# Optimization experiments

Hardware: AMD Instinct MI355X
Metric: run time of the kernel (lower is better)

The kernel has to match this reference:

```python
import jax, jax.numpy as jnp
import numpy as np

ITERATIONS = 20  # Resonator(iterations=20)
B, F, V, D = 128, 4, 2048, 4096


def _hardsign(x):
    # bipolar normalization used by MAP-VSA multiset(normalize=True); ties -> +1
    return jnp.where(x >= 0, 1.0, -1.0).astype(x.dtype)


def setup_inputs() -> dict:
    key = jax.random.key(0)
    k1, k2 = jax.random.split(key, 2)
    # bipolar codebooks: (F, V, D)
    codebooks = _hardsign(jax.random.normal(k1, (F, V, D), dtype=jnp.float32))
    # a realistic composite input: bind (elementwise product) of one codevector per factor
    idx = jax.random.randint(k2, (B, F), 0, V)                       # (B, F)
    chosen = codebooks[jnp.arange(F)[None, :], idx]                  # (B, F, D)
    inputs = jnp.prod(chosen, axis=1)                                # (B, D)
    # standard resonator init: normalized superposition of each codebook
    init_estimates = jnp.broadcast_to(
        _hardsign(jnp.sum(codebooks, axis=1)), (B, F, D)
    ).astype(jnp.float32)                                            # (B, F, D)
    return {"inputs": inputs, "init_estimates": init_estimates, "codebooks": codebooks}


def _resonator_step(inputs, est, codebooks):
    # est: (B, F, D). rolled stack over k=1..F-1 -> (B, F, F-1, D)
    f = est.shape[-2]
    rolled = jnp.stack([jnp.roll(est, k, axis=-2) for k in range(1, f)], axis=-2)
    inv_others = jnp.prod(rolled, axis=-2)          # multibind over dim -2 -> (B, F, D)
    new_est = inputs[:, None, :] * inv_others       # bind -> (B, F, D)
    sim = jnp.einsum('bfd,fvd->bfv', new_est, codebooks)   # similarity (activation='NONE')
    # multiset(codebooks, sim, normalize=True)
    return _hardsign(jnp.einsum('bfv,fvd->bfd', sim, codebooks))


def reference(inputs, init_estimates, codebooks):
    def body(carry, i):
        est, k, done = carry
        new = _resonator_step(inputs, est, codebooks)
        eq = jnp.all(new == est)          # convergence check (fixed point)
        k = jnp.where(done, k, i)
        return (new, k, done | eq), None

    carry0 = (init_estimates, jnp.int32(0), jnp.bool_(False))
    (est, k, _), _ = jax.lax.scan(body, carry0, jnp.arange(ITERATIONS, dtype=jnp.int32))
    # cleanup: argmax of |similarity| per factor (argmax_abs=True)
    sim = jnp.einsum('bfd,fvd->bfv', est, codebooks)
    outcome = jnp.argmax(jnp.abs(sim), axis=-1)     # (B, F) int indices
    return outcome, k
```

## Files before the change

kernel.cpp:

```cpp
#include <hip/hip_runtime.h>
#include <stdint.h>

#define B_    128
#define F_    4
#define V_    2048
#define D_    4096
#define DW    64
#define VW    32
#define ITERS 20
#define NKT   16

typedef _Float16 half8 __attribute__((ext_vector_type(8)));
typedef float   floatx4 __attribute__((ext_vector_type(4)));

__device__ __forceinline__ void pack16(const float* __restrict__ x,
                                       uint64_t* __restrict__ bits, int t) {
    const float4* p = (const float4*)x + (size_t)t * 4;
    uint32_t m = 0;
    #pragma unroll
    for (int j = 0; j < 4; ++j) {
        float4 v = p[j];
        m |= (__float_as_uint(v.x) >> 31) << (4 * j + 0);
        m |= (__float_as_uint(v.y) >> 31) << (4 * j + 1);
        m |= (__float_as_uint(v.z) >> 31) << (4 * j + 2);
        m |= (__float_as_uint(v.w) >> 31) << (4 * j + 3);
    }
    ((unsigned short*)bits)[t] = (unsigned short)m;
}

__global__ __launch_bounds__(256) void k_setup(
        const float* __restrict__ cb, const float* __restrict__ inite,
        const float* __restrict__ inputs,
        uint64_t* __restrict__ cb_bits, uint64_t* __restrict__ est_bits,
        uint64_t* __restrict__ in_bits,
        int* __restrict__ flags, int* __restrict__ keys) {
    int gtid = blockIdx.x * 256 + threadIdx.x;
    const int T = 512 * 256;
    const int ncb = (F_ * V_ * D_) / 16;
    for (int t = gtid; t < ncb; t += T) pack16(cb, cb_bits, t);
    pack16(inite, est_bits, gtid);
    if (gtid < (B_ * D_) / 16) pack16(inputs, in_bits, gtid);
    if (gtid < 32) flags[gtid] = 0;
    if (gtid < B_ * F_) keys[gtid] = 0;
}

__global__ void k_packT(const uint64_t* __restrict__ cb_bits,
                        uint64_t* __restrict__ cbT) {
    int vw = blockIdx.x, dwg = blockIdx.y, f = blockIdx.z;
    int lane = threadIdx.x & 63;
    int dw = dwg * 4 + (threadIdx.x >> 6);
    uint64_t w = cb_bits[((size_t)f * V_ + vw * 64 + lane) * DW + dw];
    uint64_t r = 0;
    for (int d2 = 0; d2 < 64; ++d2) {
        uint64_t m = __ballot((unsigned)((w >> d2) & 1));
        if (lane == d2) r = m;
    }
    cbT[((size_t)f * D_ + dw * 64 + lane) * VW + vw] = r;
}

__global__ __launch_bounds__(256) void k_sim(
        const uint64_t* __restrict__ cb_bits,
        const uint64_t* __restrict__ in_bits,
        const uint64_t* __restrict__ est_bits,
        _Float16* __restrict__ simf,
        const int* __restrict__ flags, int iter) {
    if (iter > 0 && flags[iter - 1] == 0) return;
    int vt = blockIdx.x, bt = blockIdx.y, f = blockIdx.z;
    int v0 = vt * 64, b0 = bt * 32;
    int tid = threadIdx.x;

    __shared__ __align__(16) ulonglong2 CB2[64 * 32];
    __shared__ __align__(16) ulonglong2 NB2[32 * 32];

    #pragma unroll
    for (int it = 0; it < 8; ++it) {
        int cq = it * 256 + tid;
        int r = cq >> 5, ch = cq & 31;
        const ulonglong2* src = (const ulonglong2*)(cb_bits + ((size_t)f * V_ + v0 + r) * DW);
        CB2[r * 32 + (ch ^ (r & 7))] = src[ch];
    }
    #pragma unroll
    for (int it = 0; it < 4; ++it) {
        int cq = it * 256 + tid;
        int r = cq >> 5, ch = cq & 31;
        int b = b0 + r;
        const ulonglong2* iv = (const ulonglong2*)(in_bits + (size_t)b * DW);
        const uint64_t* eb = est_bits + (size_t)b * F_ * DW;
        ulonglong2 i2 = iv[ch];
        ulonglong2 e0 = ((const ulonglong2*)(eb + 0 * DW))[ch];
        ulonglong2 e1 = ((const ulonglong2*)(eb + 1 * DW))[ch];
        ulonglong2 e2 = ((const ulonglong2*)(eb + 2 * DW))[ch];
        ulonglong2 e3 = ((const ulonglong2*)(eb + 3 * DW))[ch];
        ulonglong2 es = ((const ulonglong2*)(eb + (size_t)f * DW))[ch];
        ulonglong2 val;
        val.x = i2.x ^ e0.x ^ e1.x ^ e2.x ^ e3.x ^ es.x;
        val.y = i2.y ^ e0.y ^ e1.y ^ e2.y ^ e3.y ^ es.y;
        NB2[r * 32 + (ch ^ (r & 7))] = val;
    }
    __syncthreads();

    int vv = tid & 15, bb = tid >> 4;
    int svz = vv & 7, sbz = bb & 7;
    int pc[2][4];
    #pragma unroll
    for (int j = 0; j < 2; ++j)
        #pragma unroll
        for (int i = 0; i < 4; ++i) pc[j][i] = 0;

    #pragma unroll 4
    for (int ch = 0; ch < 32; ++ch) {
        ulonglong2 c[4], n[2];
        #pragma unroll
        for (int i = 0; i < 4; ++i)
            c[i] = CB2[(vv + 16 * i) * 32 + (ch ^ svz)];
        #pragma unroll
        for (int j = 0; j < 2; ++j)
            n[j] = NB2[(bb + 16 * j) * 32 + (ch ^ sbz)];
        #pragma unroll
        for (int j = 0; j < 2; ++j)
            #pragma unroll
            for (int i = 0; i < 4; ++i)
                pc[j][i] += __popcll(n[j].x ^ c[i].x) + __popcll(n[j].y ^ c[i].y);
    }
    #pragma unroll
    for (int j = 0; j < 2; ++j) {
        int b = b0 + bb + 16 * j;
        #pragma unroll
        for (int i = 0; i < 4; ++i) {
            int v = v0 + vv + 16 * i;
            simf[((size_t)f * B_ + b) * V_ + v] = (_Float16)(2048 - pc[j][i]);
        }
    }
}

__global__ __launch_bounds__(256) void k_gemm(
        const _Float16* __restrict__ simf,
        const uint64_t* __restrict__ cbT,
        uint64_t* __restrict__ est_bits,
        int* __restrict__ flags, int iter) {
    if (iter > 0 && flags[iter - 1] == 0) return;
    int nt = blockIdx.x, mt = blockIdx.y, f = blockIdx.z;
    int m0 = mt * 64, n0 = nt * 64;
    int tid = threadIdx.x;
    int lane = tid & 63, wave = tid >> 6;
    int lrow = lane & 15, lq = lane >> 4;
    int wm = wave & 1, wn = wave >> 1;

    __shared__ __align__(16) uint64_t Bb[64 * VW];
    __shared__ __align__(16) _Float16 As[64 * 128];
    __shared__ int bd;
    if (tid == 0) bd = 0;

    const uint64_t* bsrc = cbT + ((size_t)f * D_ + n0) * VW;
    #pragma unroll
    for (int p = 0; p < 4; ++p) {
        int chunk = p * 256 + tid;
        int dloc = chunk >> 4, cw = chunk & 15;
        ulonglong2 val = *(const ulonglong2*)&bsrc[dloc * VW + cw * 2];
        *(ulonglong2*)&Bb[dloc * VW + ((cw ^ (dloc & 15)) * 2)] = val;
    }

    const _Float16* Ab = simf + (size_t)f * B_ * V_ + (size_t)m0 * V_;
    int arow = tid >> 4, acol = tid & 15;
    half8 areg[4];
    #pragma unroll
    for (int p = 0; p < 4; ++p)
        areg[p] = *(const half8*)&Ab[(size_t)(p * 16 + arow) * V_ + acol * 8];

    floatx4 acc[2][2] = {};

    const uint64_t SPREAD = 0x1000200040008000ull;
    const uint64_t SMASK  = 0x8000800080008000ull;
    const uint64_t PONE   = 0x3C003C003C003C00ull;

    #pragma unroll 1
    for (int kt = 0; kt < NKT; ++kt) {
        __syncthreads();
        #pragma unroll
        for (int p = 0; p < 4; ++p)
            *(half8*)&As[(p * 16 + arow) * 128 + ((acol ^ arow) * 8)] = areg[p];
        if (kt + 1 < NKT) {
            #pragma unroll
            for (int p = 0; p < 4; ++p)
                areg[p] = *(const half8*)&Ab[(size_t)(p * 16 + arow) * V_ + (kt + 1) * 128 + acol * 8];
        }
        __syncthreads();

        ulonglong2 bw[2];
        #pragma unroll
        for (int nt2 = 0; nt2 < 2; ++nt2) {
            int dloc = wn * 32 + nt2 * 16 + lrow;
            bw[nt2] = *(const ulonglong2*)&Bb[dloc * VW + ((kt ^ (dloc & 15)) * 2)];
        }
        #pragma unroll
        for (int ks = 0; ks < 4; ++ks) {
            half8 af[2];
            #pragma unroll
            for (int mt2 = 0; mt2 < 2; ++mt2) {
                int row = wm * 32 + mt2 * 16 + lrow;
                af[mt2] = *(const half8*)&As[row * 128 + (((ks * 4 + lq) ^ lrow) * 8)];
            }
            half8 bfrag[2];
            #pragma unroll
            for (int nt2 = 0; nt2 < 2; ++nt2) {
                uint64_t w = (ks < 2) ? bw[nt2].x : bw[nt2].y;
                uint32_t byte = (uint32_t)(w >> ((((ks & 1) * 4 + lq)) * 8)) & 0xFFu;
                union { uint64_t q[2]; half8 h; } bu;
                bu.q[0] = (((uint64_t)(byte & 0xFu) * SPREAD) & SMASK) ^ PONE;
                bu.q[1] = (((uint64_t)(byte >> 4)   * SPREAD) & SMASK) ^ PONE;
                bfrag[nt2] = bu.h;
            }
            #pragma unroll
            for (int mt2 = 0; mt2 < 2; ++mt2)
                #pragma unroll
                for (int nt2 = 0; nt2 < 2; ++nt2)
                    acc[mt2][nt2] = __builtin_amdgcn_mfma_f32_16x16x32_f16(
                        af[mt2], bfrag[nt2], acc[mt2][nt2], 0, 0, 0);
        }
    }

    __syncthreads();
    unsigned char* S = (unsigned char*)As;
    #pragma unroll
    for (int mt2 = 0; mt2 < 2; ++mt2)
        #pragma unroll
        for (int nt2 = 0; nt2 < 2; ++nt2)
            #pragma unroll
            for (int r = 0; r < 4; ++r) {
                int row = wm * 32 + mt2 * 16 + lq * 4 + r;
                int col = wn * 32 + nt2 * 16 + lrow;
                S[row * 64 + col] = (acc[mt2][nt2][r] < 0.0f) ? 1 : 0;
            }
    __syncthreads();
    if (tid < 64) {
        const uint64_t* Sw = (const uint64_t*)S;
        uint64_t m = 0;
        #pragma unroll
        for (int j = 0; j < 8; ++j) {
            uint64_t w = Sw[tid * 8 + j];
            m |= ((w * 0x0102040810204080ull) >> 56) << (8 * j);
        }
        size_t widx = ((size_t)(m0 + tid) * F_ + f) * DW + nt;
        uint64_t old = est_bits[widx];
        est_bits[widx] = m;
        if (old != m) atomicOr(&bd, 1);
    }
    __syncthreads();
    if (tid == 0 && bd) atomicOr(&flags[iter], 1);
}

__global__ __launch_bounds__(256) void k_argmax(
        const uint64_t* __restrict__ cb_bits,
        const uint64_t* __restrict__ est_bits,
        int* __restrict__ keys) {
    int vt = blockIdx.x, f = blockIdx.y;
    int v0 = vt * 32;
    int tid = threadIdx.x;

    __shared__ __align__(16) ulonglong2 EB2[128 * 32];
    __shared__ __align__(16) ulonglong2 CBa[32 * 32];

    #pragma unroll
    for (int it = 0; it < 16; ++it) {
        int cq = it * 256 + tid;
        int r = cq >> 5, ch = cq & 31;
        const ulonglong2* src = (const ulonglong2*)(est_bits + ((size_t)r * F_ + f) * DW);
        EB2[r * 32 + (ch ^ (r & 7))] = src[ch];
    }
    #pragma unroll
    for (int it = 0; it < 4; ++it) {
        int cq = it * 256 + tid;
        int r = cq >> 5, ch = cq & 31;
        const ulonglong2* src = (const ulonglong2*)(cb_bits + ((size_t)f * V_ + v0 + r) * DW);
        CBa[r * 32 + (ch ^ (r & 7))] = src[ch];
    }
    __syncthreads();

    int vv = tid & 15, bb = tid >> 4;
    int svz = vv & 7, sbz = bb & 7;
    int pc[8][2];
    #pragma unroll
    for (int j = 0; j < 8; ++j) { pc[j][0] = 0; pc[j][1] = 0; }

    #pragma unroll 4
    for (int ch = 0; ch < 32; ++ch) {
        ulonglong2 c[2], n[8];
        #pragma unroll
        for (int i = 0; i < 2; ++i)
            c[i] = CBa[(vv + 16 * i) * 32 + (ch ^ svz)];
        #pragma unroll
        for (int j = 0; j < 8; ++j)
            n[j] = EB2[(bb + 16 * j) * 32 + (ch ^ sbz)];
        #pragma unroll
        for (int j = 0; j < 8; ++j)
            #pragma unroll
            for (int i = 0; i < 2; ++i)
                pc[j][i] += __popcll(n[j].x ^ c[i].x) + __popcll(n[j].y ^ c[i].y);
    }

    #pragma unroll
    for (int j = 0; j < 8; ++j) {
        int kj = (int)0x80000000;
        #pragma unroll
        for (int i = 0; i < 2; ++i) {
            int v = v0 + vv + 16 * i;
            int m = 2048 - pc[j][i]; if (m < 0) m = -m;
            int key = (m << 11) | (2047 - v);
            if (key > kj) kj = key;
        }
        #pragma unroll
        for (int s = 1; s < 16; s <<= 1) {
            int o = __shfl_xor(kj, s, 64);
            if (o > kj) kj = o;
        }
        if ((tid & 15) == 0)
            atomicMax(&keys[(size_t)(bb + 16 * j) * F_ + f], kj);
    }
}

__global__ void k_final(const int* __restrict__ keys, const int* __restrict__ flags,
                        int* __restrict__ out) {
    int tid = blockIdx.x * blockDim.x + threadIdx.x;
    if (tid < B_ * F_) out[tid] = 2047 - (keys[tid] & 0x7FF);
    if (tid == 0) {
        int k = ITERS - 1;
        for (int i = 0; i < ITERS; ++i) if (flags[i] == 0) { k = i; break; }
        out[B_ * F_] = k;
    }
}

extern "C" void kernel_launch(void* const* d_in, const int* in_sizes, int n_in,
                              void* d_out, int out_size, void* d_ws, size_t ws_size,
                              hipStream_t stream) {
    const float* inputs = (const float*)d_in[0];
    const float* inite  = (const float*)d_in[1];
    const float* cb     = (const float*)d_in[2];
    int* out = (int*)d_out;

    char* ws = (char*)d_ws;
    uint64_t* cb_bits  = (uint64_t*)ws;  ws += (size_t)F_ * V_ * DW * 8;
    uint64_t* cbT_bits = (uint64_t*)ws;  ws += (size_t)F_ * D_ * VW * 8;
    uint64_t* est_bits = (uint64_t*)ws;  ws += (size_t)B_ * F_ * DW * 8;
    uint64_t* in_bits  = (uint64_t*)ws;  ws += (size_t)B_ * DW * 8;
    _Float16* simf     = (_Float16*)ws;  ws += (size_t)F_ * B_ * V_ * 2;
    int*      flags    = (int*)ws;       ws += 32 * 4;
    int*      keys     = (int*)ws;       ws += B_ * F_ * 4;

    k_setup<<<512, 256, 0, stream>>>(cb, inite, inputs, cb_bits, est_bits,
                                     in_bits, flags, keys);
    k_packT<<<dim3(32, 16, 4), 256, 0, stream>>>(cb_bits, cbT_bits);

    for (int i = 0; i < ITERS; ++i) {
        k_sim<<<dim3(32, 4, 4), 256, 0, stream>>>(cb_bits, in_bits, est_bits, simf, flags, i);
        k_gemm<<<dim3(64, 2, 4), 256, 0, stream>>>(simf, cbT_bits, est_bits, flags, i);
    }
    k_argmax<<<dim3(64, 4), 256, 0, stream>>>(cb_bits, est_bits, keys);
    k_final<<<2, 256, 0, stream>>>(keys, flags, out);
}
```

Measured before the change: 950.4 us.

## Fuse resonator iterations into one persistent kernel with grid-wide barriers

Replaces the 40 per-iteration launches of the similarity and GEMM kernels with a single persistent kernel of 512 blocks. The blocks synchronise between phases through a hierarchical atomic-counter grid barrier. Shared estimate and similarity buffers are read and written with relaxed agent-scope atomics for cross-block visibility. This removes kernel launch gaps, but the per-iteration convergence early-exit is dropped and the spin barrier depends on all blocks being co-resident. The barrier also has a spin cap that could break synchronisation.

New measurement: 965.8 us. Within noise of the previous version (+1.6%).

```diff
diff --git a/kernel.cpp b/kernel.cpp
--- a/kernel.cpp
+++ b/kernel.cpp
@@ -9,9 +9,47 @@
 #define VW    32
 #define ITERS 20
 #define NKT   16
+#define NBLK  512
 
 typedef _Float16 half8 __attribute__((ext_vector_type(8)));
 typedef float   floatx4 __attribute__((ext_vector_type(4)));
+
+__device__ __forceinline__ uint64_t cload64(const uint64_t* p) {
+    return __hip_atomic_load(p, __ATOMIC_RELAXED, __HIP_MEMORY_SCOPE_AGENT);
+}
+__device__ __forceinline__ void cstore64(uint64_t* p, uint64_t v) {
+    __hip_atomic_store(p, v, __ATOMIC_RELAXED, __HIP_MEMORY_SCOPE_AGENT);
+}
+__device__ __forceinline__ ulonglong2 cload_u128(const uint64_t* p) {
+    ulonglong2 r;
+    r.x = cload64(p); r.y = cload64(p + 1);
+    return r;
+}
+__device__ __forceinline__ half8 cload_h8(const _Float16* p) {
+    union { uint64_t q[2]; half8 h; } u;
+    u.q[0] = cload64((const uint64_t*)p);
+    u.q[1] = cload64((const uint64_t*)p + 1);
+    return u.h;
+}
+
+__device__ __forceinline__ void xbar(int* bar, int gen) {
+    __syncthreads();
+    if (threadIdx.x == 0) {
+        int s = blockIdx.x & 15;
+        int t = __hip_atomic_fetch_add(&bar[s * 16], 1, __ATOMIC_RELAXED,
+                                       __HIP_MEMORY_SCOPE_AGENT);
+        if (t == gen * (NBLK / 16) - 1)
+            __hip_atomic_fetch_add(&bar[256], 1, __ATOMIC_RELAXED,
+                                   __HIP_MEMORY_SCOPE_AGENT);
+        int spins = 0;
+        while (__hip_atomic_load(&bar[256], __ATOMIC_RELAXED,
+                                 __HIP_MEMORY_SCOPE_AGENT) < gen * 16) {
+            __builtin_amdgcn_s_sleep(2);
+            if (++spins > (1 << 16)) break;
+        }
+    }
+    __syncthreads();
+}
 
 __device__ __forceinline__ void pack16(const float* __restrict__ x,
                                        uint64_t* __restrict__ bits, int t) {
@@ -58,195 +96,205 @@
     cbT[((size_t)f * D_ + dw * 64 + lane) * VW + vw] = r;
 }
 
-__global__ __launch_bounds__(256) void k_sim(
-        const uint64_t* __restrict__ cb_bits,
-        const uint64_t* __restrict__ in_bits,
-        const uint64_t* __restrict__ est_bits,
-        _Float16* __restrict__ simf,
-        const int* __restrict__ flags, int iter) {
-    if (iter > 0 && flags[iter - 1] == 0) return;
-    int vt = blockIdx.x, bt = blockIdx.y, f = blockIdx.z;
-    int v0 = vt * 64, b0 = bt * 32;
-    int tid = threadIdx.x;
-
-    __shared__ __align__(16) ulonglong2 CB2[64 * 32];
-    __shared__ __align__(16) ulonglong2 NB2[32 * 32];
-
-    #pragma unroll
-    for (int it = 0; it < 8; ++it) {
-        int cq = it * 256 + tid;
-        int r = cq >> 5, ch = cq & 31;
-        const ulonglong2* src = (const ulonglong2*)(cb_bits + ((size_t)f * V_ + v0 + r) * DW);
-        CB2[r * 32 + (ch ^ (r & 7))] = src[ch];
-    }
-    #pragma unroll
-    for (int it = 0; it < 4; ++it) {
-        int cq = it * 256 + tid;
-        int r = cq >> 5, ch = cq & 31;
-        int b = b0 + r;
-        const ulonglong2* iv = (const ulonglong2*)(in_bits + (size_t)b * DW);
-        const uint64_t* eb = est_bits + (size_t)b * F_ * DW;
-        ulonglong2 i2 = iv[ch];
-        ulonglong2 e0 = ((const ulonglong2*)(eb + 0 * DW))[ch];
-        ulonglong2 e1 = ((const ulonglong2*)(eb + 1 * DW))[ch];
-        ulonglong2 e2 = ((const ulonglong2*)(eb + 2 * DW))[ch];
-        ulonglong2 e3 = ((const ulonglong2*)(eb + 3 * DW))[ch];
-        ulonglong2 es = ((const ulonglong2*)(eb + (size_t)f * DW))[ch];
-        ulonglong2 val;
-        val.x = i2.x ^ e0.x ^ e1.x ^ e2.x ^ e3.x ^ es.x;
-        val.y = i2.y ^ e0.y ^ e1.y ^ e2.y ^ e3.y ^ es.y;
-        NB2[r * 32 + (ch ^ (r & 7))] = val;
-    }
-    __syncthreads();
-
-    int vv = tid & 15, bb = tid >> 4;
-    int svz = vv & 7, sbz = bb & 7;
-    int pc[2][4];
-    #pragma unroll
-    for (int j = 0; j < 2; ++j)
-        #pragma unroll
-        for (int i = 0; i < 4; ++i) pc[j][i] = 0;
-
-    #pragma unroll 4
-    for (int ch = 0; ch < 32; ++ch) {
-        ulonglong2 c[4], n[2];
-        #pragma unroll
-        for (int i = 0; i < 4; ++i)
-            c[i] = CB2[(vv + 16 * i) * 32 + (ch ^ svz)];
-        #pragma unroll
-        for (int j = 0; j < 2; ++j)
-            n[j] = NB2[(bb + 16 * j) * 32 + (ch ^ sbz)];
-        #pragma unroll
-        for (int j = 0; j < 2; ++j)
-            #pragma unroll
-            for (int i = 0; i < 4; ++i)
-                pc[j][i] += __popcll(n[j].x ^ c[i].x) + __popcll(n[j].y ^ c[i].y);
-    }
-    #pragma unroll
-    for (int j = 0; j < 2; ++j) {
-        int b = b0 + bb + 16 * j;
-        #pragma unroll
-        for (int i = 0; i < 4; ++i) {
-            int v = v0 + vv + 16 * i;
-            simf[((size_t)f * B_ + b) * V_ + v] = (_Float16)(2048 - pc[j][i]);
+__global__ __launch_bounds__(256, 2) void k_loop(
+        const uint64_t* __restrict__ cb_bits, const uint64_t* __restrict__ cbT,
+        uint64_t* __restrict__ est_bits, const uint64_t* __restrict__ in_bits,
+        _Float16* __restrict__ simf, int* __restrict__ flags, int* bar) {
+    const int bid = blockIdx.x;
+    const int tid = threadIdx.x;
+    int g = 0;
+
+    __shared__ __align__(16) unsigned char LDSU[49152];
+    __shared__ int bd;
+
+    #pragma unroll 1
+    for (int i = 0; i < ITERS; ++i) {
+        {
+            int vt = bid & 31, bt = (bid >> 5) & 3, f = bid >> 7;
+            int v0 = vt * 64, b0 = bt * 32;
+            ulonglong2* CB2 = (ulonglong2*)LDSU;
+            ulonglong2* NB2 = (ulonglong2*)(LDSU + 32768);
+            #pragma unroll
+            for (int it = 0; it < 8; ++it) {
+                int cq = it * 256 + tid;
+                int r = cq >> 5, ch = cq & 31;
+                const ulonglong2* src = (const ulonglong2*)(cb_bits + ((size_t)f * V_ + v0 + r) * DW);
+                CB2[r * 32 + (ch ^ (r & 7))] = src[ch];
+            }
+            #pragma unroll
+            for (int it = 0; it < 4; ++it) {
+                int cq = it * 256 + tid;
+                int r = cq >> 5, ch = cq & 31;
+                int b = b0 + r;
+                const ulonglong2* iv = (const ulonglong2*)(in_bits + (size_t)b * DW);
+                const uint64_t* eb = est_bits + (size_t)b * F_ * DW;
+                ulonglong2 i2 = iv[ch];
+                ulonglong2 e0 = cload_u128(eb + 0 * DW + 2 * ch);
+                ulonglong2 e1 = cload_u128(eb + 1 * DW + 2 * ch);
+                ulonglong2 e2 = cload_u128(eb + 2 * DW + 2 * ch);
+                ulonglong2 e3 = cload_u128(eb + 3 * DW + 2 * ch);
+                uint64_t ex = (f == 0) ? e0.x : (f == 1) ? e1.x : (f == 2) ? e2.x : e3.x;
+                uint64_t ey = (f == 0) ? e0.y : (f == 1) ? e1.y : (f == 2) ? e2.y : e3.y;
+                ulonglong2 val;
+                val.x = i2.x ^ e0.x ^ e1.x ^ e2.x ^ e3.x ^ ex;
+                val.y = i2.y ^ e0.y ^ e1.y ^ e2.y ^ e3.y ^ ey;
+                NB2[r * 32 + (ch ^ (r & 7))] = val;
+            }
+            __syncthreads();
+
+            int vv = tid & 15, bb = tid >> 4;
+            int svz = vv & 7, sbz = bb & 7;
+            int pc[2][4];
+            #pragma unroll
+            for (int j = 0; j < 2; ++j)
+                #pragma unroll
+                for (int ii = 0; ii < 4; ++ii) pc[j][ii] = 0;
+
+            #pragma unroll 4
+            for (int ch = 0; ch < 32; ++ch) {
+                ulonglong2 c[4], n[2];
+                #pragma unroll
+                for (int ii = 0; ii < 4; ++ii)
+                    c[ii] = CB2[(vv + 16 * ii) * 32 + (ch ^ svz)];
+                #pragma unroll
+                for (int j = 0; j < 2; ++j)
+                    n[j] = NB2[(bb + 16 * j) * 32 + (ch ^ sbz)];
+                #pragma unroll
+                for (int j = 0; j < 2; ++j)
+                    #pragma unroll
+                    for (int ii = 0; ii < 4; ++ii)
+                        pc[j][ii] += __popcll(n[j].x ^ c[ii].x) + __popcll(n[j].y ^ c[ii].y);
+            }
+            #pragma unroll
+            for (int j = 0; j < 2; ++j) {
+                int b = b0 + bb + 16 * j;
+                #pragma unroll
+                for (int ii = 0; ii < 4; ++ii) {
+                    int v = v0 + vv + 16 * ii;
+                    union { _Float16 hf; unsigned short us; } cv;
+                    cv.hf = (_Float16)(2048 - pc[j][ii]);
+                    int other = __shfl_xor((int)cv.us, 1, 64);
+                    if (!(vv & 1)) {
+                        uint32_t packv = (uint32_t)cv.us | ((uint32_t)other << 16);
+                        __hip_atomic_store(
+                            (uint32_t*)&simf[((size_t)f * B_ + b) * V_ + v], packv,
+                            __ATOMIC_RELAXED, __HIP_MEMORY_SCOPE_AGENT);
+                    }
+                }
+            }
         }
-    }
-}
-
-__global__ __launch_bounds__(256) void k_gemm(
-        const _Float16* __restrict__ simf,
-        const uint64_t* __restrict__ cbT,
-        uint64_t* __restrict__ est_bits,
-        int* __restrict__ flags, int iter) {
-    if (iter > 0 && flags[iter - 1] == 0) return;
-    int nt = blockIdx.x, mt = blockIdx.y, f = blockIdx.z;
-    int m0 = mt * 64, n0 = nt * 64;
-    int tid = threadIdx.x;
-    int lane = tid & 63, wave = tid >> 6;
-    int lrow = lane & 15, lq = lane >> 4;
-    int wm = wave & 1, wn = wave >> 1;
-
-    __shared__ __align__(16) uint64_t Bb[64 * VW];
-    __shared__ __align__(16) _Float16 As[64 * 128];
-    __shared__ int bd;
-    if (tid == 0) bd = 0;
-
-    const uint64_t* bsrc = cbT + ((size_t)f * D_ + n0) * VW;
-    #pragma unroll
-    for (int p = 0; p < 4; ++p) {
-        int chunk = p * 256 + tid;
-        int dloc = chunk >> 4, cw = chunk & 15;
-        ulonglong2 val = *(const ulonglong2*)&bsrc[dloc * VW + cw * 2];
-        *(ulonglong2*)&Bb[dloc * VW + ((cw ^ (dloc & 15)) * 2)] = val;
-    }
-
-    const _Float16* Ab = simf + (size_t)f * B_ * V_ + (size_t)m0 * V_;
-    int arow = tid >> 4, acol = tid & 15;
-    half8 areg[4];
-    #pragma unroll
-    for (int p = 0; p < 4; ++p)
-        areg[p] = *(const half8*)&Ab[(size_t)(p * 16 + arow) * V_ + acol * 8];
-
-    floatx4 acc[2][2] = {};
-
-    const uint64_t SPREAD = 0x1000200040008000ull;
-    const uint64_t SMASK  = 0x8000800080008000ull;
-    const uint64_t PONE   = 0x3C003C003C003C00ull;
-
-    #pragma unroll 1
-    for (int kt = 0; kt < NKT; ++kt) {
-        __syncthreads();
-        #pragma unroll
-        for (int p = 0; p < 4; ++p)
-            *(half8*)&As[(p * 16 + arow) * 128 + ((acol ^ arow) * 8)] = areg[p];
-        if (kt + 1 < NKT) {
+        xbar(bar, ++g);
+
+        {
+            int gnt = bid & 63, gmt = (bid >> 6) & 1, gf = bid >> 7;
+            int m0 = gmt * 64, n0 = gnt * 64;
+            int lane = tid & 63, wave = tid >> 6;
+            int lrow = lane & 15, lq = lane >> 4;
+            int wm = wave & 1, wn = wave >> 1;
+
+            uint64_t* Bb = (uint64_t*)LDSU;
+            _Float16* As = (_Float16*)(LDSU + 16384);
+            if (tid == 0) bd = 0;
+
+            const uint64_t* bsrc = cbT + ((size_t)gf * D_ + n0) * VW;
+            #pragma unroll
+            for (int p = 0; p < 4; ++p) {
+                int chunk = p * 256 + tid;
+                int dloc = chunk >> 4, cw = chunk & 15;
+                ulonglong2 val = *(const ulonglong2*)&bsrc[dloc * VW + cw * 2];
+                *(ulonglong2*)&Bb[dloc * VW + ((cw ^ (dloc & 15)) * 2)] = val;
+            }
+
+            const _Float16* Ab = simf + (size_t)gf * B_ * V_ + (size_t)m0 * V_;
+            int arow = tid >> 4, acol = tid & 15;
+            half8 areg[4];
             #pragma unroll
             for (int p = 0; p < 4; ++p)
-                areg[p] = *(const half8*)&Ab[(size_t)(p * 16 + arow) * V_ + (kt + 1) * 128 + acol * 8];
+                areg[p] = cload_h8(&Ab[(size_t)(p * 16 + arow) * V_ + acol * 8]);
+
+            floatx4 acc[2][2] = {};
+
+            const uint64_t SPREAD = 0x1000200040008000ull;
+            const uint64_t SMASK  = 0x8000800080008000ull;
+            const uint64_t PONE   = 0x3C003C003C003C00ull;
+
+            #pragma unroll 1
+            for (int kt = 0; kt < NKT; ++kt) {
+                __syncthreads();
+                #pragma unroll
+                for (int p = 0; p < 4; ++p)
+                    *(half8*)&As[(p * 16 + arow) * 128 + ((acol ^ arow) * 8)] = areg[p];
+                if (kt + 1 < NKT) {
+                    #pragma unroll
+                    for (int p = 0; p < 4; ++p)
+                        areg[p] = cload_h8(&Ab[(size_t)(p * 16 + arow) * V_ + (kt + 1) * 128 + acol * 8]);
+                }
+                __syncthreads();
+
+                ulonglong2 bw[2];
+                #pragma unroll
+                for (int nt2 = 0; nt2 < 2; ++nt2) {
+                    int dloc = wn * 32 + nt2 * 16 + lrow;
+                    bw[nt2] = *(const ulonglong2*)&Bb[dloc * VW + ((kt ^ (dloc & 15)) * 2)];
+                }
+                #pragma unroll
+                for (int ks = 0; ks < 4; ++ks) {
+                    half8 af[2];
+                    #pragma unroll
+                    for (int mt2 = 0; mt2 < 2; ++mt2) {
+                        int row = wm * 32 + mt2 * 16 + lrow;
+                        af[mt2] = *(const half8*)&As[row * 128 + (((ks * 4 + lq) ^ lrow) * 8)];
+                    }
+                    half8 bfrag[2];
+                    #pragma unroll
+                    for (int nt2 = 0; nt2 < 2; ++nt2) {
+                        uint64_t w = (ks < 2) ? bw[nt2].x : bw[nt2].y;
+                        uint32_t byte = (uint32_t)(w >> ((((ks & 1) * 4 + lq)) * 8)) & 0xFFu;
+                        union { uint64_t q[2]; half8 h; } bu;
+                        bu.q[0] = (((uint64_t)(byte & 0xFu) * SPREAD) & SMASK) ^ PONE;
+                        bu.q[1] = (((uint64_t)(byte >> 4)   * SPREAD) & SMASK) ^ PONE;
+                        bfrag[nt2] = bu.h;
+                    }
+                    #pragma unroll
+                    for (int mt2 = 0; mt2 < 2; ++mt2)
+                        #pragma unroll
+                        for (int nt2 = 0; nt2 < 2; ++nt2)
+                            acc[mt2][nt2] = __builtin_amdgcn_mfma_f32_16x16x32_f16(
+                                af[mt2], bfrag[nt2], acc[mt2][nt2], 0, 0, 0);
+                }
+            }
+
+            __syncthreads();
+            unsigned char* S = (unsigned char*)As;
+            #pragma unroll
+            for (int mt2 = 0; mt2 < 2; ++mt2)
+                #pragma unroll
+                for (int nt2 = 0; nt2 < 2; ++nt2)
+                    #pragma unroll
+                    for (int r = 0; r < 4; ++r) {
+                        int row = wm * 32 + mt2 * 16 + lq * 4 + r;
+                        int col = wn * 32 + nt2 * 16 + lrow;
+                        S[row * 64 + col] = (acc[mt2][nt2][r] < 0.0f) ? 1 : 0;
+                    }
+            __syncthreads();
+            if (tid < 64) {
+                const uint64_t* Sw = (const uint64_t*)S;
+                uint64_t m = 0;
+                #pragma unroll
+                for (int j = 0; j < 8; ++j) {
+                    uint64_t w = Sw[tid * 8 + j];
+                    m |= ((w * 0x0102040810204080ull) >> 56) << (8 * j);
+                }
+                size_t widx = ((size_t)(m0 + tid) * F_ + gf) * DW + gnt;
+                uint64_t old = cload64(&est_bits[widx]);
+                cstore64(&est_bits[widx], m);
+                if (old != m) atomicOr(&bd, 1);
+            }
+            __syncthreads();
+            if (tid == 0 && bd) atomicOr(&flags[i], 1);
         }
-        __syncthreads();
-
-        ulonglong2 bw[2];
-        #pragma unroll
-        for (int nt2 = 0; nt2 < 2; ++nt2) {
-            int dloc = wn * 32 + nt2 * 16 + lrow;
-            bw[nt2] = *(const ulonglong2*)&Bb[dloc * VW + ((kt ^ (dloc & 15)) * 2)];
-        }
-        #pragma unroll
-        for (int ks = 0; ks < 4; ++ks) {
-            half8 af[2];
-            #pragma unroll
-            for (int mt2 = 0; mt2 < 2; ++mt2) {
-                int row = wm * 32 + mt2 * 16 + lrow;
-                af[mt2] = *(const half8*)&As[row * 128 + (((ks * 4 + lq) ^ lrow) * 8)];
-            }
-            half8 bfrag[2];
-            #pragma unroll
-            for (int nt2 = 0; nt2 < 2; ++nt2) {
-                uint64_t w = (ks < 2) ? bw[nt2].x : bw[nt2].y;
-                uint32_t byte = (uint32_t)(w >> ((((ks & 1) * 4 + lq)) * 8)) & 0xFFu;
-                union { uint64_t q[2]; half8 h; } bu;
-                bu.q[0] = (((uint64_t)(byte & 0xFu) * SPREAD) & SMASK) ^ PONE;
-                bu.q[1] = (((uint64_t)(byte >> 4)   * SPREAD) & SMASK) ^ PONE;
-                bfrag[nt2] = bu.h;
-            }
-            #pragma unroll
-            for (int mt2 = 0; mt2 < 2; ++mt2)
-                #pragma unroll
-                for (int nt2 = 0; nt2 < 2; ++nt2)
-                    acc[mt2][nt2] = __builtin_amdgcn_mfma_f32_16x16x32_f16(
-                        af[mt2], bfrag[nt2], acc[mt2][nt2], 0, 0, 0);
-        }
-    }
-
-    __syncthreads();
-    unsigned char* S = (unsigned char*)As;
-    #pragma unroll
-    for (int mt2 = 0; mt2 < 2; ++mt2)
-        #pragma unroll
-        for (int nt2 = 0; nt2 < 2; ++nt2)
-            #pragma unroll
-            for (int r = 0; r < 4; ++r) {
-                int row = wm * 32 + mt2 * 16 + lq * 4 + r;
-                int col = wn * 32 + nt2 * 16 + lrow;
-                S[row * 64 + col] = (acc[mt2][nt2][r] < 0.0f) ? 1 : 0;
-            }
-    __syncthreads();
-    if (tid < 64) {
-        const uint64_t* Sw = (const uint64_t*)S;
-        uint64_t m = 0;
-        #pragma unroll
-        for (int j = 0; j < 8; ++j) {
-            uint64_t w = Sw[tid * 8 + j];
-            m |= ((w * 0x0102040810204080ull) >> 56) << (8 * j);
-        }
-        size_t widx = ((size_t)(m0 + tid) * F_ + f) * DW + nt;
-        uint64_t old = est_bits[widx];
-        est_bits[widx] = m;
-        if (old != m) atomicOr(&bd, 1);
-    }
-    __syncthreads();
-    if (tid == 0 && bd) atomicOr(&flags[iter], 1);
+        if (i + 1 < ITERS) xbar(bar, ++g);
+    }
 }
 
 __global__ __launch_bounds__(256) void k_argmax(
@@ -345,15 +393,15 @@
     _Float16* simf     = (_Float16*)ws;  ws += (size_t)F_ * B_ * V_ * 2;
     int*      flags    = (int*)ws;       ws += 32 * 4;
     int*      keys     = (int*)ws;       ws += B_ * F_ * 4;
+    int*      bar      = (int*)ws;       ws += 2048;
+
+    hipMemsetAsync(bar, 0, 2048, stream);
 
     k_setup<<<512, 256, 0, stream>>>(cb, inite, inputs, cb_bits, est_bits,
                                      in_bits, flags, keys);
     k_packT<<<dim3(32, 16, 4), 256, 0, stream>>>(cb_bits, cbT_bits);
-
-    for (int i = 0; i < ITERS; ++i) {
-        k_sim<<<dim3(32, 4, 4), 256, 0, stream>>>(cb_bits, in_bits, est_bits, simf, flags, i);
-        k_gemm<<<dim3(64, 2, 4), 256, 0, stream>>>(simf, cbT_bits, est_bits, flags, i);
-    }
+    k_loop<<<NBLK, 256, 0, stream>>>(cb_bits, cbT_bits, est_bits, in_bits,
+                                     simf, flags, bar);
     k_argmax<<<dim3(64, 4), 256, 0, stream>>>(cb_bits, est_bits, keys);
     k_final<<<2, 256, 0, stream>>>(keys, flags, out);
 }
```
